# Kernel optimization log

Measured on AMD Instinct MI355X. Metric: run time of the kernel, lower is better.

Reference implementation:

```python
import jax, jax.numpy as jnp
import numpy as np

TIM_SIZE, TIM_EMB = 48, 64
APP_SIZE, APP_EMB = 10000, 256
UID_SIZE, UID_EMB = 10000, 256
INPUT_SIZE = TIM_EMB + APP_EMB  # 320
S = 4096
N = S - 3  # windows of length 4


def setup_inputs() -> dict:
    key = jax.random.key(0)
    ks = jax.random.split(key, 12)
    inp = {
        "tim": jax.random.randint(ks[0], (S, 1), 0, TIM_SIZE),
        "app": jax.random.uniform(ks[1], (S, APP_SIZE), dtype=jnp.float32),
        "loc": jax.random.randint(ks[2], (S, 1), 0, 1),
        "uid": jax.random.randint(ks[3], (1,), 0, UID_SIZE),
        "ptim": jax.random.randint(ks[4], (N, 1), 0, TIM_SIZE),
        # learned parameters
        "emb_tim_w": jax.random.normal(ks[5], (TIM_SIZE, TIM_EMB), dtype=jnp.float32) * 0.02,
        "emb_uid_w": jax.random.normal(ks[6], (UID_SIZE, UID_EMB), dtype=jnp.float32) * 0.02,
        "emb_app_w": jax.random.normal(ks[7], (APP_SIZE, APP_EMB), dtype=jnp.float32) * 0.02,
        "attn_W": jax.random.uniform(ks[8], (INPUT_SIZE, 1), dtype=jnp.float32),
        "attn_b": jax.random.uniform(ks[9], (4, 1), dtype=jnp.float32),
        "attn_fc_w": jax.random.normal(ks[10], (APP_EMB, INPUT_SIZE), dtype=jnp.float32) * 0.02,
        "attn_fc_b": jnp.zeros((APP_EMB,), dtype=jnp.float32),
        "dec_w": jax.random.normal(ks[11], (APP_SIZE, APP_EMB + TIM_EMB), dtype=jnp.float32) * 0.02,
        "dec_b": jnp.zeros((APP_SIZE,), dtype=jnp.float32),
    }
    return inp


def reference(tim, app, loc, uid, ptim, emb_tim_w, emb_uid_w, emb_app_w,
              attn_W, attn_b, attn_fc_w, attn_fc_b, dec_w, dec_b):
    # embeddings (squeeze(1) in torch)
    tim_emb = emb_tim_w[tim[:, 0]]    # [S, TIM_EMB]
    ptim_emb = emb_tim_w[ptim[:, 0]]  # [N, TIM_EMB]
    # 'sum' app embedding mode: multi-hot @ table
    app_emb = app @ emb_app_w         # [S, APP_EMB]
    x = jnp.concatenate([app_emb, tim_emb], axis=1)  # [S, INPUT_SIZE]; dropout is identity at eval
    # sliding windows of length 4 (vectorizes the torch per-i loop)
    n = tim.shape[0] - 3
    idx = jnp.arange(n)[:, None] + jnp.arange(4)[None, :]  # [N, 4]
    win = x[idx]                                          # [N, 4, INPUT_SIZE]
    H = jnp.tanh(win @ attn_W + attn_b)                   # [N, 4, 1]
    Xn = H / jnp.sum(jnp.abs(H), axis=(1, 2), keepdims=True)  # L1 normalize over the window
    pooled = jnp.einsum('nf,nfd->nd', Xn[:, :, 0], win)   # [N, INPUT_SIZE]
    out = pooled @ attn_fc_w.T + attn_fc_b                # [N, APP_EMB]
    uid_emb = emb_uid_w[uid[0]]                           # [APP_EMB], broadcast = repeat
    out = out * uid_emb
    out = jnp.concatenate([out, ptim_emb], axis=1)        # [N, APP_EMB+TIM_EMB]
    score = jax.nn.sigmoid(out @ dec_w.T + dec_b)         # [N, APP_SIZE]
    return score
```

## Files before the change

### kernel.cpp

```cpp
#include <hip/hip_runtime.h>

typedef __attribute__((ext_vector_type(8))) short  bf16x8;
typedef __attribute__((ext_vector_type(8))) unsigned short u16x8;
typedef __attribute__((ext_vector_type(4))) float  f32x4;

constexpr int S    = 4096;
constexpr int NR   = 4093;
constexpr int KAPP = 10000;
constexpr int EAPP = 256;
constexpr int ETIM = 64;
constexpr int DIN  = 320;
constexpr int NDEC = 10000;
constexpr int NSK  = 8;
constexpr int KCH  = 1280;
constexpr int CH   = 320;
constexpr int NCH  = KCH / CH;
constexpr int KPAD = 10240;

__device__ inline unsigned short f2bf(float f) {
    unsigned u = __float_as_uint(f);
    u += 0x7fffu + ((u >> 16) & 1u);
    return (unsigned short)(u >> 16);
}
__device__ inline float bf2f(unsigned short h) {
    return __uint_as_float(((unsigned)h) << 16);
}
__device__ inline u16x8 pack8(f32x4 a, f32x4 b) {
    u16x8 v;
    v[0]=f2bf(a.x); v[1]=f2bf(a.y); v[2]=f2bf(a.z); v[3]=f2bf(a.w);
    v[4]=f2bf(b.x); v[5]=f2bf(b.y); v[6]=f2bf(b.z); v[7]=f2bf(b.w);
    return v;
}
__device__ inline bf16x8 as_bf(u16x8 v) {
    union { u16x8 u; bf16x8 b; } c; c.u = v; return c.b;
}

__global__ __launch_bounds__(256) void k_cvt_bf16(
    const float* __restrict__ in, unsigned short* __restrict__ out, int n8)
{
    int id = blockIdx.x * 256 + threadIdx.x;
    if (id >= n8) return;
    const float* p = in + (size_t)id * 8;
    f32x4 a = *reinterpret_cast<const f32x4*>(p);
    f32x4 b = *reinterpret_cast<const f32x4*>(p + 4);
    *reinterpret_cast<u16x8*>(out + (size_t)id * 8) = pack8(a, b);
}

__global__ __launch_bounds__(256) void k_transpose_appw(
    const float* __restrict__ B, unsigned short* __restrict__ Bp)
{
    __shared__ float T[64][68];
    const int kt = blockIdx.x * 64, nt = blockIdx.y * 64;
    const int tid = threadIdx.x;
    #pragma unroll
    for (int i = 0; i < 4; ++i) {
        int c = tid + (i << 8);
        int k = c >> 4, n4 = (c & 15) << 2;
        f32x4 v = {0.f, 0.f, 0.f, 0.f};
        if (kt + k < KAPP)
            v = *reinterpret_cast<const f32x4*>(&B[(size_t)(kt + k) * EAPP + nt + n4]);
        *reinterpret_cast<f32x4*>(&T[k][n4]) = v;
    }
    __syncthreads();
    #pragma unroll
    for (int i = 0; i < 2; ++i) {
        int c = tid + (i << 8);
        int n = c >> 3, ko = (c & 7) << 3;
        u16x8 v;
        #pragma unroll
        for (int j = 0; j < 8; ++j) v[j] = f2bf(T[ko + j][n]);
        *reinterpret_cast<u16x8*>(&Bp[(size_t)(nt + n) * KPAD + kt + ko]) = v;
    }
}

__global__ __launch_bounds__(256) void k_embed_tim(
    const int* __restrict__ tim, const float* __restrict__ emb_tim,
    unsigned short* __restrict__ xb)
{
    int r = blockIdx.x * 4 + (threadIdx.x >> 6);
    int e = threadIdx.x & 63;
    xb[(size_t)r * DIN + EAPP + e] = f2bf(emb_tim[tim[r] * ETIM + e]);
}
__global__ __launch_bounds__(256) void k_embed_ptim(
    const int* __restrict__ ptim, const float* __restrict__ emb_tim,
    unsigned short* __restrict__ yb)
{
    int r = blockIdx.x * 4 + (threadIdx.x >> 6);
    int e = threadIdx.x & 63;
    if (r < NR) yb[(size_t)r * DIN + EAPP + e] = f2bf(emb_tim[ptim[r] * ETIM + e]);
}

__global__ __launch_bounds__(256, 2) void k_app(
    const float* __restrict__ A, const unsigned short* __restrict__ Bp,
    float* __restrict__ part)
{
    __shared__ unsigned short As[40 * 128 * 8];
    const int tid = threadIdx.x, lane = tid & 63, w = tid >> 6;
    const int ks = blockIdx.x, bm = blockIdx.y << 7;
    const int wc = w << 6, rl = lane & 15, kq = lane >> 4;

    f32x4 acc[8][4];
    #pragma unroll
    for (int i = 0; i < 8; ++i)
        #pragma unroll
        for (int j = 0; j < 4; ++j) acc[i][j] = (f32x4){0.f, 0.f, 0.f, 0.f};

    u16x8 b0[4], b1[4];

#define LOADB(DST, KB, KSN) do {                                                \
    const int kg_ = (KB) + ((KSN) << 5) + (kq << 3);                            \
    _Pragma("unroll")                                                           \
    for (int j = 0; j < 4; ++j) {                                               \
        int brow = wc + j * 16 + rl;                                            \
        DST[j] = *reinterpret_cast<const u16x8*>(                               \
            &Bp[(size_t)brow * KPAD + kg_]);                                    \
    }                                                                           \
} while (0)

#define STEP(BARR, KSN) do {                                                    \
    const int ckb_ = ((KSN) << 2) + kq;                                         \
    bf16x8 af_[8];                                                              \
    _Pragma("unroll")                                                           \
    for (int i = 0; i < 8; ++i)                                                 \
        af_[i] = *reinterpret_cast<const bf16x8*>(                              \
            &As[((ckb_ << 7) + (i << 4) + rl) << 3]);                           \
    _Pragma("unroll")                                                           \
    for (int i = 0; i < 8; ++i)                                                 \
        _Pragma("unroll")                                                       \
        for (int j = 0; j < 4; ++j)                                             \
            acc[i][j] = __builtin_amdgcn_mfma_f32_16x16x32_bf16(                \
                af_[i], as_bf(BARR[j]), acc[i][j], 0, 0, 0);                     \
} while (0)

    for (int c = 0; c < NCH; ++c) {
        const int kb = ks * KCH + c * CH;
        __syncthreads();
        {
            const int row = tid >> 1, half = tid & 1;
            const float* src = A + (size_t)(bm + row) * KAPP + kb;
            #pragma unroll
            for (int t = 0; t < 20; ++t) {
                int ck = half + (t << 1);
                u16x8 v = {0,0,0,0,0,0,0,0};
                if (kb + (ck << 3) + 8 <= KAPP) {
                    const float* p = src + (ck << 3);
                    v = pack8(*reinterpret_cast<const f32x4*>(p),
                              *reinterpret_cast<const f32x4*>(p + 4));
                }
                *reinterpret_cast<u16x8*>(&As[((ck << 7) + row) << 3]) = v;
            }
        }
        __syncthreads();

        LOADB(b0, kb, 0);
        LOADB(b1, kb, 1);
        #pragma unroll
        for (int p = 0; p < 5; ++p) {
            STEP(b0, 2 * p);
            if (2 * p + 2 < 10) LOADB(b0, kb, 2 * p + 2);
            STEP(b1, 2 * p + 1);
            if (2 * p + 3 < 10) LOADB(b1, kb, 2 * p + 3);
        }
    }
#undef LOADB
#undef STEP

    float* P = part + ((size_t)ks * S + bm) * EAPP;
    const int rq = kq << 2;
    #pragma unroll
    for (int i = 0; i < 8; ++i)
        #pragma unroll
        for (int j = 0; j < 4; ++j) {
            int col = wc + j * 16 + rl;
            #pragma unroll
            for (int q = 0; q < 4; ++q)
                __builtin_nontemporal_store(acc[i][j][q],
                    &P[(size_t)(i * 16 + rq + q) * EAPP + col]);
        }
}

__global__ __launch_bounds__(256) void k_reduce_app(
    const float* __restrict__ part, unsigned short* __restrict__ xb)
{
    int id = blockIdx.x * 256 + threadIdx.x;
    int row = id >> 6, c4 = (id & 63) << 2;
    f32x4 s = {0.f, 0.f, 0.f, 0.f};
    #pragma unroll
    for (int sl = 0; sl < NSK; ++sl) {
        f32x4 v = __builtin_nontemporal_load(reinterpret_cast<const f32x4*>(
            &part[((size_t)sl * S + row) * EAPP + c4]));
        s.x += v.x; s.y += v.y; s.z += v.z; s.w += v.w;
    }
    unsigned short* o = &xb[(size_t)row * DIN + c4];
    o[0] = f2bf(s.x); o[1] = f2bf(s.y); o[2] = f2bf(s.z); o[3] = f2bf(s.w);
}

__global__ __launch_bounds__(256) void k_score(
    const unsigned short* __restrict__ xb, const float* __restrict__ W,
    float* __restrict__ s)
{
    int wv = threadIdx.x >> 6, lane = threadIdx.x & 63;
    int m = blockIdx.x * 4 + wv;
    float sum = 0.f;
    #pragma unroll
    for (int i = 0; i < 5; ++i) {
        int k = lane + (i << 6);
        sum += bf2f(xb[(size_t)m * DIN + k]) * W[k];
    }
    #pragma unroll
    for (int off = 32; off; off >>= 1) sum += __shfl_down(sum, off);
    if (lane == 0) s[m] = sum;
}

__global__ void k_pooled(
    const unsigned short* __restrict__ xb, const float* __restrict__ s,
    const float* __restrict__ attn_b, unsigned short* __restrict__ pooledb)
{
    int n = blockIdx.x, d = threadIdx.x;
    float h[4], den = 0.f;
    #pragma unroll
    for (int f = 0; f < 4; ++f) {
        h[f] = tanhf(s[n + f] + attn_b[f]);
        den += fabsf(h[f]);
    }
    float inv = 1.f / den, p = 0.f;
    #pragma unroll
    for (int f = 0; f < 4; ++f)
        p = fmaf(h[f] * inv, bf2f(xb[(size_t)(n + f) * DIN + d]), p);
    pooledb[(size_t)n * DIN + d] = f2bf(p);
}

template<int EPI>
__global__ __launch_bounds__(256, 4) void k_nt320(
    const unsigned short* __restrict__ A, const unsigned short* __restrict__ B,
    int Nb, int Mlim,
    const float* __restrict__ bias,
    const float* __restrict__ emb_uid, const int* __restrict__ uid,
    void* __restrict__ Cout, int ldc)
{
    __shared__ unsigned short As[40 * 64 * 8];
    const int tid = threadIdx.x, lane = tid & 63, w = tid >> 6;
    const int qx = gridDim.x >> 3;
    const int swz = (blockIdx.x & 7) * qx + (blockIdx.x >> 3);
    const int nbn = (Nb + 255) >> 8;
    const int bm = (swz / nbn) << 6, bn = (swz % nbn) << 8;
    const int rl = lane & 15, kq = lane >> 4;
    const int wc = w << 6;

    {
        const int row = tid >> 2, c0 = tid & 3;
        const unsigned short* src = A + (size_t)(bm + row) * DIN;
        #pragma unroll
        for (int t = 0; t < 10; ++t) {
            int ck = c0 + (t << 2);
            *reinterpret_cast<u16x8*>(&As[((ck << 6) + row) << 3]) =
                *reinterpret_cast<const u16x8*>(src + (ck << 3));
        }
    }
    __syncthreads();

    f32x4 acc[4][4];
    #pragma unroll
    for (int i = 0; i < 4; ++i)
        #pragma unroll
        for (int j = 0; j < 4; ++j) acc[i][j] = (f32x4){0.f, 0.f, 0.f, 0.f};

    u16x8 b0[4], b1[4];
#define LOADB(DST, KSN) do {                                                    \
    const int kg_ = ((KSN) << 5) + (kq << 3);                                   \
    _Pragma("unroll")                                                           \
    for (int j = 0; j < 4; ++j) {                                               \
        int brow = bn + wc + j * 16 + rl;                                       \
        u16x8 v_ = {0,0,0,0,0,0,0,0};                                           \
        if (brow < Nb)                                                          \
            v_ = *reinterpret_cast<const u16x8*>(&B[(size_t)brow * DIN + kg_]); \
        DST[j] = v_;                                                            \
    }                                                                           \
} while (0)

#define STEPNT(BARR, KSN) do {                                                  \
    const int ckb_ = (((KSN) << 2) + kq) << 6;                                  \
    bf16x8 af_[4];                                                              \
    _Pragma("unroll")                                                           \
    for (int i = 0; i < 4; ++i)                                                 \
        af_[i] = *reinterpret_cast<const bf16x8*>(                              \
            &As[(ckb_ + i * 16 + rl) << 3]);                                    \
    _Pragma("unroll")                                                           \
    for (int i = 0; i < 4; ++i)                                                 \
        _Pragma("unroll")                                                       \
        for (int j = 0; j < 4; ++j)                                             \
            acc[i][j] = __builtin_amdgcn_mfma_f32_16x16x32_bf16(                \
                af_[i], as_bf(BARR[j]), acc[i][j], 0, 0, 0);                     \
} while (0)

    LOADB(b0, 0);
    LOADB(b1, 1);
    #pragma unroll
    for (int p = 0; p < 5; ++p) {
        STEPNT(b0, 2 * p);
        if (2 * p + 2 < 10) LOADB(b0, 2 * p + 2);
        STEPNT(b1, 2 * p + 1);
        if (2 * p + 3 < 10) LOADB(b1, 2 * p + 3);
    }
#undef LOADB
#undef STEPNT

    const int rq = kq << 2;
    if (EPI == 1) {
        unsigned short* C = (unsigned short*)Cout;
        const float* us = emb_uid + (size_t)uid[0] * EAPP;
        #pragma unroll
        for (int j = 0; j < 4; ++j) {
            int col = bn + wc + j * 16 + rl;
            if (col >= Nb) continue;
            float um = us[col], bb = bias[col];
            #pragma unroll
            for (int i = 0; i < 4; ++i)
                #pragma unroll
                for (int q = 0; q < 4; ++q) {
                    int row = bm + i * 16 + rq + q;
                    if (row < Mlim)
                        C[(size_t)row * ldc + col] = f2bf((acc[i][j][q] + bb) * um);
                }
        }
    } else {
        float* C = (float*)Cout;
        float* epi = reinterpret_cast<float*>(As);
        float bb[4];
        #pragma unroll
        for (int j = 0; j < 4; ++j) {
            int col = bn + wc + j * 16 + rl;
            bb[j] = (col < Nb) ? bias[col] : 0.f;
        }
        const int r16 = tid >> 6, c4 = (tid & 63) << 2;
        #pragma unroll
        for (int i = 0; i < 4; ++i) {
            __syncthreads();
            #pragma unroll
            for (int j = 0; j < 4; ++j) {
                int colL = wc + j * 16 + rl;
                #pragma unroll
                for (int q = 0; q < 4; ++q) {
                    float v = acc[i][j][q] + bb[j];
                    epi[(rq + q) * 260 + colL] = 1.f / (1.f + __expf(-v));
                }
            }
            __syncthreads();
            #pragma unroll
            for (int r4 = 0; r4 < 4; ++r4) {
                int rowL = (r4 << 2) + r16;
                int grow = bm + (i << 4) + rowL;
                f32x4 v = *reinterpret_cast<const f32x4*>(&epi[rowL * 260 + c4]);
                if (grow < Mlim) {
                    if (bn + 256 <= Nb) {
                        __builtin_nontemporal_store(v,
                            reinterpret_cast<f32x4*>(&C[(size_t)grow * ldc + bn + c4]));
                    } else {
                        #pragma unroll
                        for (int e = 0; e < 4; ++e)
                            if (bn + c4 + e < Nb)
                                __builtin_nontemporal_store(v[e],
                                    &C[(size_t)grow * ldc + bn + c4 + e]);
                    }
                }
            }
        }
    }
}

extern "C" void kernel_launch(void* const* d_in, const int* in_sizes, int n_in,
                              void* d_out, int out_size, void* d_ws, size_t ws_size,
                              hipStream_t stream)
{
    const int*   tim       = (const int*)  d_in[0];
    const float* app       = (const float*)d_in[1];
    const int*   uid       = (const int*)  d_in[3];
    const int*   ptim      = (const int*)  d_in[4];
    const float* emb_tim_w = (const float*)d_in[5];
    const float* emb_uid_w = (const float*)d_in[6];
    const float* emb_app_w = (const float*)d_in[7];
    const float* attn_W    = (const float*)d_in[8];
    const float* attn_b    = (const float*)d_in[9];
    const float* attn_fc_w = (const float*)d_in[10];
    const float* attn_fc_b = (const float*)d_in[11];
    const float* dec_w     = (const float*)d_in[12];
    const float* dec_b     = (const float*)d_in[13];
    float* out = (float*)d_out;

    char* w = (char*)d_ws;
    size_t o = 0;
    auto alloc = [&](size_t bytes) { char* p = w + o; o = (o + bytes + 511) & ~(size_t)511; return p; };
    unsigned short* xb      = (unsigned short*)alloc((size_t)S * DIN * 2);
    unsigned short* pooledb = (unsigned short*)alloc((size_t)S * DIN * 2);
    unsigned short* yb      = (unsigned short*)alloc((size_t)S * DIN * 2);
    float*          s       = (float*)        alloc((size_t)S * 4);
    unsigned short* Bp      = (unsigned short*)alloc((size_t)EAPP * KPAD * 2);
    unsigned short* decb    = (unsigned short*)alloc((size_t)NDEC * DIN * 2);
    unsigned short* fcb     = (unsigned short*)alloc((size_t)EAPP * DIN * 2);
    float*          part    = (float*)        alloc((size_t)NSK * S * EAPP * 4);

    k_cvt_bf16<<<(NDEC * DIN / 8 + 255) / 256, 256, 0, stream>>>(dec_w, decb, NDEC * DIN / 8);
    k_cvt_bf16<<<(EAPP * DIN / 8 + 255) / 256, 256, 0, stream>>>(attn_fc_w, fcb, EAPP * DIN / 8);
    dim3 gT(KPAD / 64, EAPP / 64);
    k_transpose_appw<<<gT, 256, 0, stream>>>(emb_app_w, Bp);
    k_embed_tim<<<S / 4, 256, 0, stream>>>(tim, emb_tim_w, xb);

    dim3 gApp(NSK, S / 128);
    k_app<<<gApp, 256, 0, stream>>>(app, Bp, part);
    k_reduce_app<<<S * 64 / 256, 256, 0, stream>>>(part, xb);

    k_score<<<S / 4, 256, 0, stream>>>(xb, attn_W, s);
    k_pooled<<<NR, DIN, 0, stream>>>(xb, s, attn_b, pooledb);
    k_embed_ptim<<<S / 4, 256, 0, stream>>>(ptim, emb_tim_w, yb);

    k_nt320<1><<<64, 256, 0, stream>>>(pooledb, fcb, EAPP, S,
                                       attn_fc_b, emb_uid_w, uid, yb, DIN);
    k_nt320<2><<<40 * 64, 256, 0, stream>>>(yb, decb, NDEC, NR,
                                            dec_b, nullptr, nullptr, out, NDEC);
}
```

Baseline: 223.4 us.

## Prefetch next A chunk into registers during MFMA in app GEMM, shrink tiles

The app-embedding GEMM now loads the next K chunk of the fp32 multi-hot matrix into registers while the current chunk's MFMAs run, then converts it to bf16 and writes it to shared memory. The M tile is halved to 64 rows, giving twice as many blocks. The K chunk drops to 256, and the shared-memory layout uses an XOR swizzle to cut bank conflicts. The aim is to hide global-load latency on the large A stream and raise occupancy, at the cost of higher register pressure. Each B fragment is also reused across fewer rows.

```diff
diff --git a/kernel.cpp b/kernel.cpp
--- a/kernel.cpp
+++ b/kernel.cpp
@@ -2,6 +2,7 @@
 
 typedef __attribute__((ext_vector_type(8))) short  bf16x8;
 typedef __attribute__((ext_vector_type(8))) unsigned short u16x8;
+typedef __attribute__((ext_vector_type(4))) unsigned short u16x4;
 typedef __attribute__((ext_vector_type(4))) float  f32x4;
 
 constexpr int S    = 4096;
@@ -13,7 +14,7 @@
 constexpr int NDEC = 10000;
 constexpr int NSK  = 8;
 constexpr int KCH  = 1280;
-constexpr int CH   = 320;
+constexpr int CH   = 256;
 constexpr int NCH  = KCH / CH;
 constexpr int KPAD = 10240;
 
@@ -94,18 +95,41 @@
     const float* __restrict__ A, const unsigned short* __restrict__ Bp,
     float* __restrict__ part)
 {
-    __shared__ unsigned short As[40 * 128 * 8];
+    __shared__ unsigned short As[32 * 64 * 8];
     const int tid = threadIdx.x, lane = tid & 63, w = tid >> 6;
-    const int ks = blockIdx.x, bm = blockIdx.y << 7;
+    const int ks = blockIdx.x, bm = blockIdx.y << 6;
     const int wc = w << 6, rl = lane & 15, kq = lane >> 4;
-
-    f32x4 acc[8][4];
-    #pragma unroll
-    for (int i = 0; i < 8; ++i)
+    const int k0 = ks * KCH;
+    const size_t AMAX = (size_t)S * KAPP;
+
+    f32x4 areg[16];
+    f32x4 acc[4][4];
+    #pragma unroll
+    for (int i = 0; i < 4; ++i)
         #pragma unroll
         for (int j = 0; j < 4; ++j) acc[i][j] = (f32x4){0.f, 0.f, 0.f, 0.f};
-
     u16x8 b0[4], b1[4];
+
+#define ISSUE_A(R, KB) do {                                                     \
+    size_t off_ = (size_t)(bm + (w << 4) + (R)) * KAPP + (KB) + (lane << 2);    \
+    f32x4 v_ = {0.f, 0.f, 0.f, 0.f};                                            \
+    if (off_ + 4 <= AMAX)                                                       \
+        v_ = *reinterpret_cast<const f32x4*>(A + off_);                         \
+    areg[R] = v_;                                                               \
+} while (0)
+
+#define WRITE_A() do {                                                          \
+    const int ck_ = lane >> 1, x_ = ck_ & 7, ho_ = (lane & 1) << 2;             \
+    _Pragma("unroll")                                                           \
+    for (int r = 0; r < 16; ++r) {                                              \
+        int row_ = (w << 4) + r;                                                \
+        u16x4 p_;                                                               \
+        p_[0] = f2bf(areg[r].x); p_[1] = f2bf(areg[r].y);                       \
+        p_[2] = f2bf(areg[r].z); p_[3] = f2bf(areg[r].w);                       \
+        *reinterpret_cast<u16x4*>(                                              \
+            &As[(((ck_ << 6) + (row_ ^ x_)) << 3) + ho_]) = p_;                 \
+    }                                                                           \
+} while (0)
 
 #define LOADB(DST, KB, KSN) do {                                                \
     const int kg_ = (KB) + ((KSN) << 5) + (kq << 3);                            \
@@ -118,57 +142,51 @@
 } while (0)
 
 #define STEP(BARR, KSN) do {                                                    \
-    const int ckb_ = ((KSN) << 2) + kq;                                         \
-    bf16x8 af_[8];                                                              \
-    _Pragma("unroll")                                                           \
-    for (int i = 0; i < 8; ++i)                                                 \
+    const int ckb_ = ((KSN) << 2) + kq, x_ = ckb_ & 7;                          \
+    bf16x8 af_[4];                                                              \
+    _Pragma("unroll")                                                           \
+    for (int i = 0; i < 4; ++i)                                                 \
         af_[i] = *reinterpret_cast<const bf16x8*>(                              \
-            &As[((ckb_ << 7) + (i << 4) + rl) << 3]);                           \
-    _Pragma("unroll")                                                           \
-    for (int i = 0; i < 8; ++i)                                                 \
+            &As[((ckb_ << 6) + (((i << 4) + rl) ^ x_)) << 3]);                  \
+    _Pragma("unroll")                                                           \
+    for (int i = 0; i < 4; ++i)                                                 \
         _Pragma("unroll")                                                       \
         for (int j = 0; j < 4; ++j)                                             \
             acc[i][j] = __builtin_amdgcn_mfma_f32_16x16x32_bf16(                \
                 af_[i], as_bf(BARR[j]), acc[i][j], 0, 0, 0);                     \
 } while (0)
 
+    #pragma unroll
+    for (int r = 0; r < 16; ++r)
+        ISSUE_A(r, k0);
     for (int c = 0; c < NCH; ++c) {
-        const int kb = ks * KCH + c * CH;
+        const int kb  = k0 + c * CH;
+        const int kbn = kb + CH;
+        const bool more = (c + 1 < NCH);
         __syncthreads();
-        {
-            const int row = tid >> 1, half = tid & 1;
-            const float* src = A + (size_t)(bm + row) * KAPP + kb;
-            #pragma unroll
-            for (int t = 0; t < 20; ++t) {
-                int ck = half + (t << 1);
-                u16x8 v = {0,0,0,0,0,0,0,0};
-                if (kb + (ck << 3) + 8 <= KAPP) {
-                    const float* p = src + (ck << 3);
-                    v = pack8(*reinterpret_cast<const f32x4*>(p),
-                              *reinterpret_cast<const f32x4*>(p + 4));
-                }
-                *reinterpret_cast<u16x8*>(&As[((ck << 7) + row) << 3]) = v;
-            }
-        }
+        WRITE_A();
         __syncthreads();
-
         LOADB(b0, kb, 0);
         LOADB(b1, kb, 1);
         #pragma unroll
-        for (int p = 0; p < 5; ++p) {
+        for (int p = 0; p < 4; ++p) {
+            if (more) { ISSUE_A(4 * p + 0, kbn); ISSUE_A(4 * p + 1, kbn); }
             STEP(b0, 2 * p);
-            if (2 * p + 2 < 10) LOADB(b0, kb, 2 * p + 2);
+            if (2 * p + 2 < 8) LOADB(b0, kb, 2 * p + 2);
+            if (more) { ISSUE_A(4 * p + 2, kbn); ISSUE_A(4 * p + 3, kbn); }
             STEP(b1, 2 * p + 1);
-            if (2 * p + 3 < 10) LOADB(b1, kb, 2 * p + 3);
-        }
-    }
+            if (2 * p + 3 < 8) LOADB(b1, kb, 2 * p + 3);
+        }
+    }
+#undef ISSUE_A
+#undef WRITE_A
 #undef LOADB
 #undef STEP
 
     float* P = part + ((size_t)ks * S + bm) * EAPP;
     const int rq = kq << 2;
     #pragma unroll
-    for (int i = 0; i < 8; ++i)
+    for (int i = 0; i < 4; ++i)
         #pragma unroll
         for (int j = 0; j < 4; ++j) {
             int col = wc + j * 16 + rl;
@@ -405,7 +423,7 @@
     k_transpose_appw<<<gT, 256, 0, stream>>>(emb_app_w, Bp);
     k_embed_tim<<<S / 4, 256, 0, stream>>>(tim, emb_tim_w, xb);
 
-    dim3 gApp(NSK, S / 128);
+    dim3 gApp(NSK, S / 64);
     k_app<<<gApp, 256, 0, stream>>>(app, Bp, part);
     k_reduce_app<<<S * 64 / 256, 256, 0, stream>>>(part, xb);
 
```

New measurement: 246.0 us. 1.1x slower.
